# Kernel tuning notes

Hardware: AMD Instinct MI355X
Metric: run time of the kernel (lower is better)

## Reference

```python
import jax, jax.numpy as jnp
import numpy as np

B, S, D = 16, 512, 768      # batch, max_n_words, context_dim (input_size)
E, R = 128, 2048            # entities per doc, candidate relations per doc
H = 768                     # config.hidden_size
H2 = H // 2                 # 384
OUT = 2                     # binary relation classes


def _linear_params(k, fan_in, fan_out):
    k1, k2 = jax.random.split(k)
    bound = 1.0 / np.sqrt(fan_in)
    W = jax.random.uniform(k1, (fan_in, fan_out), minval=-bound, maxval=bound, dtype=jnp.float32)
    b = jax.random.uniform(k2, (fan_out,), minval=-bound, maxval=bound, dtype=jnp.float32)
    return W, b


def setup_inputs() -> dict:
    key = jax.random.key(0)
    ks = jax.random.split(key, 16)
    hW1, hb1 = _linear_params(ks[0], 2 * D, H)
    hW2, hb2 = _linear_params(ks[1], H, H2)
    tW1, tb1 = _linear_params(ks[2], 2 * D, H)
    tW2, tb2 = _linear_params(ks[3], H, H2)
    bnd = 1.0 / np.sqrt(H2)
    bil_w = jax.random.uniform(ks[4], (OUT, H2, H2), minval=-bnd, maxval=bnd, dtype=jnp.float32)
    lW, lb = _linear_params(ks[5], 2 * H2, OUT)
    emb = jax.random.normal(ks[6], (3, D), dtype=jnp.float32)  # entity_emb
    hidden_states = jax.random.normal(ks[7], (B, S, D), dtype=jnp.float32)
    ent_start = jax.random.randint(ks[8], (B, E), 0, S)
    ent_label = jax.random.randint(ks[9], (B, E), 0, 3)
    rel_head = jax.random.randint(ks[10], (B, R), 0, E)
    rel_tail = jax.random.randint(ks[11], (B, R), 0, E)
    rel_label = jax.random.randint(ks[12], (B, R), 0, 2)
    return dict(hidden_states=hidden_states, emb=emb,
                hW1=hW1, hb1=hb1, hW2=hW2, hb2=hb2,
                tW1=tW1, tb1=tb1, tW2=tW2, tb2=tb2,
                bil_w=bil_w, lW=lW, lb=lb,
                ent_start=ent_start, ent_label=ent_label,
                rel_head=rel_head, rel_tail=rel_tail, rel_label=rel_label)


def reference(hidden_states, emb, hW1, hb1, hW2, hb2, tW1, tb1, tW2, tb2,
              bil_w, lW, lb, ent_start, ent_label, rel_head, rel_tail, rel_label):
    def tower(rel_idx, W1, b1, W2, b2):
        start = jnp.take_along_axis(ent_start, rel_idx, axis=1)              # [B,R]
        lab = jnp.take_along_axis(ent_label, rel_idx, axis=1)                # [B,R]
        hid = jnp.take_along_axis(hidden_states, start[..., None], axis=1)   # [B,R,D]
        rep = jnp.concatenate([hid, emb[lab]], axis=-1)                      # [B,R,2D]
        h = jax.nn.relu(rep @ W1 + b1)                                       # [B,R,H]
        return jax.nn.relu(h @ W2 + b2)                                      # [B,R,H2]

    heads = tower(rel_head, hW1, hb1, hW2, hb2)
    tails = tower(rel_tail, tW1, tb1, tW2, tb2)
    # Biaffine: bilinear (no bias) + linear over concat
    logits = (jnp.einsum('bri,oij,brj->bro', heads, bil_w, tails)
              + jnp.concatenate([heads, tails], axis=-1) @ lW + lb)          # [B,R,2]
    logp = jax.nn.log_softmax(logits, axis=-1)
    loss = -jnp.mean(jnp.take_along_axis(logp, rel_label[..., None], axis=-1))
    return loss, logits
```

## Files before the change

### kernel.cpp

```cpp
#include <hip/hip_runtime.h>
#include <hip/hip_bf16.h>
#include <cstdint>

typedef unsigned short ushort_t;
typedef __bf16 bf16x8 __attribute__((ext_vector_type(8)));
typedef float f32x4 __attribute__((ext_vector_type(4)));

#define B_   16
#define S_   512
#define D_   768
#define E_   128
#define R_   2048
#define NREL 32768

__device__ inline ushort_t f2b(float f) {
    uint32_t u = __builtin_bit_cast(uint32_t, f);
    uint32_t r = (u + 0x7fffu + ((u >> 16) & 1u)) >> 16;
    return (ushort_t)r;
}
__device__ inline float b2f(ushort_t u) {
    uint32_t v = ((uint32_t)u) << 16;
    return __builtin_bit_cast(float, v);
}
__device__ inline float bl(uint32_t u) {
    uint32_t v = u << 16;
    return __builtin_bit_cast(float, v);
}
__device__ inline float bh(uint32_t u) {
    uint32_t v = u & 0xffff0000u;
    return __builtin_bit_cast(float, v);
}

#define NB_BIAS 24
#define NB_PREP 1542

__global__ __launch_bounds__(256) void prep_fused(
    const float* __restrict__ hidden, const float* __restrict__ emb,
    const float* __restrict__ lW,
    const float* __restrict__ hW1, const float* __restrict__ tW1,
    const float* __restrict__ hW2, const float* __restrict__ tW2,
    const float* __restrict__ bil,
    const float* __restrict__ hb1, const float* __restrict__ tb1,
    const int* __restrict__ ent_start,
    ushort_t* __restrict__ repE,
    ushort_t* __restrict__ hW1T, ushort_t* __restrict__ tW1T,
    ushort_t* __restrict__ hW2T, ushort_t* __restrict__ tW2T,
    ushort_t* __restrict__ BmatT, ushort_t* __restrict__ lWtT,
    float* __restrict__ biasEh, float* __restrict__ biasEt,
    float* __restrict__ out)
{
    __shared__ float smem[3072];
    int bid = blockIdx.x;
    int tid = threadIdx.x;

    if (bid < NB_BIAS) {
        int tower = bid / 12, cb = bid - tower * 12;
        const float* W1 = tower ? tW1 : hW1;
        const float* b1 = tower ? tb1 : hb1;
        float* dstB     = tower ? biasEt : biasEh;
        int c4 = (tid & 15) * 4;
        int kg = tid >> 4;
        int col0 = cb * 64;
        const float* wp = W1 + (size_t)(768 + kg * 48) * 768 + col0 + c4;
        const float* ep = emb + kg * 48;
        float a0x = 0.f, a0y = 0.f, a0z = 0.f, a0w = 0.f;
        float a1x = 0.f, a1y = 0.f, a1z = 0.f, a1w = 0.f;
        float a2x = 0.f, a2y = 0.f, a2z = 0.f, a2w = 0.f;
#pragma unroll 8
        for (int k = 0; k < 48; ++k) {
            float4 w = *reinterpret_cast<const float4*>(wp + (size_t)k * 768);
            float e0 = ep[k], e1 = ep[768 + k], e2 = ep[1536 + k];
            a0x += e0 * w.x; a0y += e0 * w.y; a0z += e0 * w.z; a0w += e0 * w.w;
            a1x += e1 * w.x; a1y += e1 * w.y; a1z += e1 * w.z; a1w += e1 * w.w;
            a2x += e2 * w.x; a2y += e2 * w.y; a2z += e2 * w.z; a2w += e2 * w.w;
        }
        smem[kg * 192 +   0 + c4 + 0] = a0x;
        smem[kg * 192 +   0 + c4 + 1] = a0y;
        smem[kg * 192 +   0 + c4 + 2] = a0z;
        smem[kg * 192 +   0 + c4 + 3] = a0w;
        smem[kg * 192 +  64 + c4 + 0] = a1x;
        smem[kg * 192 +  64 + c4 + 1] = a1y;
        smem[kg * 192 +  64 + c4 + 2] = a1z;
        smem[kg * 192 +  64 + c4 + 3] = a1w;
        smem[kg * 192 + 128 + c4 + 0] = a2x;
        smem[kg * 192 + 128 + c4 + 1] = a2y;
        smem[kg * 192 + 128 + c4 + 2] = a2z;
        smem[kg * 192 + 128 + c4 + 3] = a2w;
        __syncthreads();
        if (tid < 192) {
            int l = tid >> 6, c = tid & 63;
            float s = 0.f;
#pragma unroll
            for (int g = 0; g < 16; ++g) s += smem[g * 192 + l * 64 + c];
            dstB[l * 768 + col0 + c] = b1[col0 + c] + s;
        }
        return;
    }

    int pb = bid - NB_BIAS;
    if (pb < NB_PREP) {
        int idx = pb * 256 + tid;
        if (idx == 0) out[0] = 0.0f;
        if (idx < 393216) {
            int row = idx / 192, q = idx - row * 192;
            int c = q * 4;
            int b = row >> 7;
            int st = ent_start[row];
            const float* srcp = hidden + ((size_t)(b * S_ + st) * D_ + c);
            float4 v = *reinterpret_cast<const float4*>(srcp);
            uint32_t lo = (uint32_t)f2b(v.x) | ((uint32_t)f2b(v.y) << 16);
            uint32_t hi = (uint32_t)f2b(v.z) | ((uint32_t)f2b(v.w) << 16);
            uint2 pk; pk.x = lo; pk.y = hi;
            *reinterpret_cast<uint2*>(repE + (size_t)idx * 4) = pk;
            return;
        }
        int i2 = idx - 393216;
        if (i2 < 768) {
            int o = i2 / 384, kk = i2 - o * 384;
            BmatT[(768 + o) * 384 + kk] = f2b(lW[kk * 2 + o]);
            return;
        }
        i2 -= 768;
        if (i2 < 768) {
            int o = i2 / 384, ii = i2 - o * 384;
            lWtT[o * 384 + ii] = f2b(lW[(384 + ii) * 2 + o]);
        }
        return;
    }

    int r = pb - NB_PREP;
    const float* src; ushort_t* dst; int Rr, Cc, xs;
    if (r < 576)        { src = hW1;          dst = hW1T;  Rr = 768; Cc = 768; xs = 24; }
    else if (r < 1152)  { r -= 576;  src = tW1;          dst = tW1T;  Rr = 768; Cc = 768; xs = 24; }
    else if (r < 1440)  { r -= 1152; src = hW2;          dst = hW2T;  Rr = 768; Cc = 384; xs = 24; }
    else if (r < 1728)  { r -= 1440; src = tW2;          dst = tW2T;  Rr = 768; Cc = 384; xs = 24; }
    else if (r < 1872)  { r -= 1728; src = bil;          dst = BmatT; Rr = 384; Cc = 384; xs = 12; }
    else                { r -= 1872; src = bil + 147456; dst = BmatT + 147456; Rr = 384; Cc = 384; xs = 12; }
    int bx = r % xs, by = r / xs;
    int tR = bx * 32, tC = by * 32;
    int tx = tid & 31, ty = tid >> 5;
#pragma unroll
    for (int rr = 0; rr < 4; ++rr)
        smem[(ty + rr * 8) * 33 + tx] = src[(size_t)(tR + ty + rr * 8) * Cc + tC + tx];
    __syncthreads();
#pragma unroll
    for (int rr = 0; rr < 4; ++rr)
        dst[(size_t)(tC + ty + rr * 8) * Rr + tR + tx] = f2b(smem[tx * 33 + ty + rr * 8]);
}

#define GLL16(src, dst) __builtin_amdgcn_global_load_lds( \
    (const __attribute__((address_space(1))) void*)(src), \
    (__attribute__((address_space(3))) void*)(dst), 16, 0, 0)

template<int BN>
__global__ __launch_bounds__(256) void gemm_lds(
    const ushort_t* __restrict__ A0, const ushort_t* __restrict__ A1,
    const ushort_t* __restrict__ Bt0, const ushort_t* __restrict__ Bt1,
    const float* __restrict__ bias0, const float* __restrict__ bias1,
    void* __restrict__ out0, void* __restrict__ out1,
    const int* __restrict__ lab,
    int M, int N0, int N1, int K, int doRelu, int f32o0, int f32o1)
{
    constexpr int NI   = BN / 32;
    constexpr int RPWB = BN / 4;
    constexpr int NSTB = RPWB / 8;
    __shared__ ushort_t As[2][4096];
    __shared__ ushort_t Bs[2][BN * 64];
    int N = blockIdx.z ? N1 : N0;
    int tileN = blockIdx.y * BN;
    if (tileN >= N) return;
    const ushort_t* A   = blockIdx.z ? A1 : A0;
    const ushort_t* Bt  = blockIdx.z ? Bt1 : Bt0;
    const float*   bias = blockIdx.z ? bias1 : bias0;
    int           f32o  = blockIdx.z ? f32o1 : f32o0;
    ushort_t*      outH = (ushort_t*)(blockIdx.z ? out1 : out0);
    float*         outF = (float*)(blockIdx.z ? out1 : out0);

    int t = threadIdx.x;
    int lane = t & 63, wave = t >> 6;
    int tileM = blockIdx.x * 64;
    int wm = (wave >> 1) * 32, wn = (wave & 1) * (BN / 2);
    int l15 = lane & 15, quad = lane >> 4;

    int grwA  = wave * 16 + (lane >> 3);
    int grwB  = wave * RPWB + (lane >> 3);
    int gseg8 = ((lane & 7) ^ (lane >> 3)) << 3;
    const ushort_t* pA = A  + (size_t)(tileM + grwA) * K + gseg8;
    const ushort_t* pB = Bt + (size_t)(tileN + grwB) * K + gseg8;
    int ldA = wave * 1024 + lane * 8;
    int ldB = wave * (RPWB * 64) + lane * 8;

    int offA[2][2], offB[NI][2];
#pragma unroll
    for (int mi = 0; mi < 2; ++mi) {
        int rw = wm + mi * 16 + l15;
#pragma unroll
        for (int ks = 0; ks < 2; ++ks)
            offA[mi][ks] = rw * 64 + (((ks * 4 + quad) ^ (rw & 7)) << 3);
    }
#pragma unroll
    for (int ni = 0; ni < NI; ++ni) {
        int rw = wn + ni * 16 + l15;
#pragma unroll
        for (int ks = 0; ks < 2; ++ks)
            offB[ni][ks] = rw * 64 + (((ks * 4 + quad) ^ (rw & 7)) << 3);
    }

    f32x4 acc[2][NI];
#pragma unroll
    for (int a = 0; a < 2; ++a)
#pragma unroll
        for (int b = 0; b < NI; ++b) {
            acc[a][b][0] = 0.f; acc[a][b][1] = 0.f;
            acc[a][b][2] = 0.f; acc[a][b][3] = 0.f;
        }

    GLL16(pA, &As[0][ldA]);
    GLL16(pA + (size_t)8 * K, &As[0][ldA + 512]);
#pragma unroll
    for (int c = 0; c < NSTB; ++c)
        GLL16(pB + (size_t)(c * 8) * K, &Bs[0][ldB + c * 512]);
    __syncthreads();

    int nk = K >> 6;
    for (int kt = 0; kt < nk; ++kt) {
        int cur = kt & 1;
        if (kt + 1 < nk) {
            int ko = (kt + 1) << 6;
            GLL16(pA + ko, &As[cur ^ 1][ldA]);
            GLL16(pA + (size_t)8 * K + ko, &As[cur ^ 1][ldA + 512]);
#pragma unroll
            for (int c = 0; c < NSTB; ++c)
                GLL16(pB + (size_t)(c * 8) * K + ko, &Bs[cur ^ 1][ldB + c * 512]);
        }
#pragma unroll
        for (int ks = 0; ks < 2; ++ks) {
            bf16x8 bfr[NI];
#pragma unroll
            for (int ni = 0; ni < NI; ++ni)
                bfr[ni] = *reinterpret_cast<const bf16x8*>(&Bs[cur][offB[ni][ks]]);
#pragma unroll
            for (int mi = 0; mi < 2; ++mi) {
                bf16x8 af = *reinterpret_cast<const bf16x8*>(&As[cur][offA[mi][ks]]);
#pragma unroll
                for (int ni = 0; ni < NI; ++ni)
                    acc[mi][ni] = __builtin_amdgcn_mfma_f32_16x16x32_bf16(af, bfr[ni], acc[mi][ni], 0, 0, 0);
            }
        }
        __syncthreads();
    }

#pragma unroll
    for (int mi = 0; mi < 2; ++mi) {
        int gr = tileM + wm + mi * 16 + quad * 4;
        int lb4[4];
        if (lab) {
#pragma unroll
            for (int r = 0; r < 4; ++r) lb4[r] = lab[gr + r];
        }
#pragma unroll
        for (int ni = 0; ni < NI; ++ni) {
            int gc = tileN + wn + ni * 16 + l15;
            if (gc < N) {
#pragma unroll
                for (int r = 0; r < 4; ++r) {
                    float bb = lab ? bias[(size_t)lb4[r] * N + gc]
                                   : (bias ? bias[gc] : 0.0f);
                    float v = acc[mi][ni][r] + bb;
                    if (doRelu) v = fmaxf(v, 0.0f);
                    if (f32o) outF[(size_t)(gr + r) * N + gc] = v;
                    else      outH[(size_t)(gr + r) * N + gc] = f2b(v);
                }
            }
        }
    }
}

__global__ __launch_bounds__(256) void rel_kernel(
    const ushort_t* __restrict__ Uext, const ushort_t* __restrict__ tailsE,
    const float* __restrict__ tLin, const float* __restrict__ lb,
    const int* __restrict__ rel_head, const int* __restrict__ rel_tail,
    const int* __restrict__ rel_label, float* __restrict__ out)
{
    __shared__ float wsum[4];
    int lane = threadIdx.x & 63, wave = threadIdx.x >> 6;
    float lb0 = lb[0], lb1 = lb[1];
    float lossAcc = 0.0f;
    int base = (blockIdx.x * 4 + wave) * 8;

    for (int q = 0; q < 8; ++q) {
        int rel = base + q;
        int b = rel >> 11;
        int h = rel_head[rel], t = rel_tail[rel], lab = rel_label[rel];
        const uint32_t* uh = reinterpret_cast<const uint32_t*>(Uext + (size_t)(b * E_ + h) * 770);
        const uint32_t* tv = reinterpret_cast<const uint32_t*>(tailsE + (size_t)(b * E_ + t) * 384);

        float a0 = 0.f, a1 = 0.f;
#pragma unroll
        for (int j = 0; j < 3; ++j) {
            int i = lane + 64 * j;
            uint32_t tu = tv[i];
            uint32_t u0 = uh[i], u1 = uh[192 + i];
            float tl = bl(tu), th = bh(tu);
            a0 += tl * bl(u0) + th * bh(u0);
            a1 += tl * bl(u1) + th * bh(u1);
        }
#pragma unroll
        for (int d = 1; d < 64; d <<= 1) {
            a0 += __shfl_xor(a0, d);
            a1 += __shfl_xor(a1, d);
        }
        const ushort_t* uhs = reinterpret_cast<const ushort_t*>(uh);
        float2 tp = reinterpret_cast<const float2*>(tLin)[b * E_ + t];
        float l0v = a0 + tp.x + b2f(uhs[768]) + lb0;
        float l1v = a1 + tp.y + b2f(uhs[769]) + lb1;
        if (lane == 0) {
            out[1 + 2 * rel]     = l0v;
            out[1 + 2 * rel + 1] = l1v;
        }
        float m = fmaxf(l0v, l1v);
        float lse = m + logf(expf(l0v - m) + expf(l1v - m));
        lossAcc += lse - (lab ? l1v : l0v);
    }
    if (lane == 0) wsum[wave] = lossAcc;
    __syncthreads();
    if (threadIdx.x == 0) {
        float s = wsum[0] + wsum[1] + wsum[2] + wsum[3];
        atomicAdd(out, s * (1.0f / 32768.0f));
    }
}

extern "C" void kernel_launch(void* const* d_in, const int* in_sizes, int n_in,
                              void* d_out, int out_size, void* d_ws, size_t ws_size,
                              hipStream_t stream)
{
    const float* hidden = (const float*)d_in[0];
    const float* emb    = (const float*)d_in[1];
    const float* hW1    = (const float*)d_in[2];
    const float* hb1    = (const float*)d_in[3];
    const float* hW2    = (const float*)d_in[4];
    const float* hb2    = (const float*)d_in[5];
    const float* tW1    = (const float*)d_in[6];
    const float* tb1    = (const float*)d_in[7];
    const float* tW2    = (const float*)d_in[8];
    const float* tb2    = (const float*)d_in[9];
    const float* bil    = (const float*)d_in[10];
    const float* lW     = (const float*)d_in[11];
    const float* lb     = (const float*)d_in[12];
    const int* ent_start = (const int*)d_in[13];
    const int* ent_label = (const int*)d_in[14];
    const int* rel_head  = (const int*)d_in[15];
    const int* rel_tail  = (const int*)d_in[16];
    const int* rel_label = (const int*)d_in[17];
    float* out = (float*)d_out;

    char* ws = (char*)d_ws;
    ushort_t* repE   = (ushort_t*)(ws + 0);
    ushort_t* hW1T   = (ushort_t*)(ws + 3145728);
    ushort_t* tW1T   = (ushort_t*)(ws + 4325376);
    ushort_t* hW2T   = (ushort_t*)(ws + 5505024);
    ushort_t* tW2T   = (ushort_t*)(ws + 6094848);
    ushort_t* BmatT  = (ushort_t*)(ws + 6684672);
    ushort_t* lWtT   = (ushort_t*)(ws + 7276032);
    float*    biasEh = (float*)   (ws + 7277568);
    float*    biasEt = (float*)   (ws + 7286784);
    float*    tLin   = (float*)   (ws + 7296000);
    ushort_t* h1     = (ushort_t*)(ws + 7312384);
    ushort_t* t1     = (ushort_t*)(ws + 10458112);
    ushort_t* headsE = (ushort_t*)(ws + 13603840);
    ushort_t* tailsE = (ushort_t*)(ws + 15176704);
    ushort_t* Uext   = (ushort_t*)(ws + 16749568);

    prep_fused<<<3582, 256, 0, stream>>>(
        hidden, emb, lW, hW1, tW1, hW2, tW2, bil, hb1, tb1, ent_start,
        repE, hW1T, tW1T, hW2T, tW2T, BmatT, lWtT, biasEh, biasEt, out);

    gemm_lds<64><<<dim3(32, 12, 2), 256, 0, stream>>>(
        repE, repE, hW1T, tW1T, biasEh, biasEt, h1, t1, ent_label,
        2048, 768, 768, 768, 1, 0, 0);

    gemm_lds<32><<<dim3(32, 12, 2), 256, 0, stream>>>(
        h1, t1, hW2T, tW2T, hb2, tb2, headsE, tailsE, nullptr,
        2048, 384, 384, 768, 1, 0, 0);

    gemm_lds<64><<<dim3(32, 13, 2), 256, 0, stream>>>(
        headsE, tailsE, BmatT, lWtT, nullptr, nullptr, Uext, tLin, nullptr,
        2048, 770, 2, 384, 0, 0, 1);

    rel_kernel<<<1024, 256, 0, stream>>>(
        Uext, tailsE, tLin, lb, rel_head, rel_tail, rel_label, out);
}
```

Measured before the change: 167.4 us.

## Triple-buffer LDS tiles with explicit vmcnt waits in GEMM

Turns the double-buffered global_load_lds pipeline into a three-stage ring that prefetches two k-tiles ahead. It replaces the full __syncthreads with partial s_waitcnt vmcnt counts plus a raw s_barrier, so loads for later tiles can stay in flight while the current tile is computed. This costs 50% more LDS per block, which may lower occupancy. The hand-set vmcnt counts must match the number of loads each stage issues for each BN.

```diff
diff --git a/kernel.cpp b/kernel.cpp
--- a/kernel.cpp
+++ b/kernel.cpp
@@ -164,8 +164,8 @@
     constexpr int NI   = BN / 32;
     constexpr int RPWB = BN / 4;
     constexpr int NSTB = RPWB / 8;
-    __shared__ ushort_t As[2][4096];
-    __shared__ ushort_t Bs[2][BN * 64];
+    __shared__ ushort_t As[3][4096];
+    __shared__ ushort_t Bs[3][BN * 64];
     int N = blockIdx.z ? N1 : N0;
     int tileN = blockIdx.y * BN;
     if (tileN >= N) return;
@@ -215,39 +215,57 @@
             acc[a][b][2] = 0.f; acc[a][b][3] = 0.f;
         }
 
-    GLL16(pA, &As[0][ldA]);
-    GLL16(pA + (size_t)8 * K, &As[0][ldA + 512]);
-#pragma unroll
-    for (int c = 0; c < NSTB; ++c)
-        GLL16(pB + (size_t)(c * 8) * K, &Bs[0][ldB + c * 512]);
-    __syncthreads();
+    auto stage = [&](int kt, int buf) {
+        int ko = kt << 6;
+        GLL16(pA + ko, &As[buf][ldA]);
+        GLL16(pA + (size_t)8 * K + ko, &As[buf][ldA + 512]);
+#pragma unroll
+        for (int c = 0; c < NSTB; ++c)
+            GLL16(pB + (size_t)(c * 8) * K + ko, &Bs[buf][ldB + c * 512]);
+    };
 
     int nk = K >> 6;
+    stage(0, 0);
+    stage(1, 1);
+    if constexpr (BN == 64) asm volatile("s_waitcnt vmcnt(4)" ::: "memory");
+    else                    asm volatile("s_waitcnt vmcnt(3)" ::: "memory");
+    __builtin_amdgcn_sched_barrier(0);
+    __builtin_amdgcn_s_barrier();
+    __builtin_amdgcn_sched_barrier(0);
+
+    int cur = 0;
     for (int kt = 0; kt < nk; ++kt) {
-        int cur = kt & 1;
-        if (kt + 1 < nk) {
-            int ko = (kt + 1) << 6;
-            GLL16(pA + ko, &As[cur ^ 1][ldA]);
-            GLL16(pA + (size_t)8 * K + ko, &As[cur ^ 1][ldA + 512]);
-#pragma unroll
-            for (int c = 0; c < NSTB; ++c)
-                GLL16(pB + (size_t)(c * 8) * K + ko, &Bs[cur ^ 1][ldB + c * 512]);
-        }
+        int pre = cur + 2; if (pre >= 3) pre -= 3;
+        if (kt + 2 < nk) stage(kt + 2, pre);
+        const ushort_t* Asc = As[cur];
+        const ushort_t* Bsc = Bs[cur];
 #pragma unroll
         for (int ks = 0; ks < 2; ++ks) {
             bf16x8 bfr[NI];
 #pragma unroll
             for (int ni = 0; ni < NI; ++ni)
-                bfr[ni] = *reinterpret_cast<const bf16x8*>(&Bs[cur][offB[ni][ks]]);
+                bfr[ni] = *reinterpret_cast<const bf16x8*>(&Bsc[offB[ni][ks]]);
 #pragma unroll
             for (int mi = 0; mi < 2; ++mi) {
-                bf16x8 af = *reinterpret_cast<const bf16x8*>(&As[cur][offA[mi][ks]]);
+                bf16x8 af = *reinterpret_cast<const bf16x8*>(&Asc[offA[mi][ks]]);
 #pragma unroll
                 for (int ni = 0; ni < NI; ++ni)
                     acc[mi][ni] = __builtin_amdgcn_mfma_f32_16x16x32_bf16(af, bfr[ni], acc[mi][ni], 0, 0, 0);
             }
         }
-        __syncthreads();
+        if (kt + 2 < nk) {
+            if constexpr (BN == 64) asm volatile("s_waitcnt vmcnt(4)" ::: "memory");
+            else                    asm volatile("s_waitcnt vmcnt(3)" ::: "memory");
+            __builtin_amdgcn_sched_barrier(0);
+            __builtin_amdgcn_s_barrier();
+            __builtin_amdgcn_sched_barrier(0);
+        } else if (kt + 1 < nk) {
+            asm volatile("s_waitcnt vmcnt(0)" ::: "memory");
+            __builtin_amdgcn_sched_barrier(0);
+            __builtin_amdgcn_s_barrier();
+            __builtin_amdgcn_sched_barrier(0);
+        }
+        cur = cur + 1; if (cur >= 3) cur -= 3;
     }
 
 #pragma unroll
```

Measured after the change: 170.6 us. No clear change (+1.9%).
